# Performance work log

Measured on AMD Instinct MI355X. Metric: run time of the kernel, lower is better.

The kernel has to match this reference:

```python
import jax, jax.numpy as jnp
import numpy as np

NQ, NK, D = 8192, 8192, 256
NEG_INF = -1e30


def setup_inputs() -> dict:
    key = jax.random.key(0)
    kK, kV, kQ, kM = jax.random.split(key, 4)
    K = jax.random.normal(kK, (NK, D), dtype=jnp.float32)
    V = jax.random.normal(kV, (NK, D), dtype=jnp.float32)
    Q = jax.random.normal(kQ, (NQ, D), dtype=jnp.float32)
    m = jax.random.randint(kM, (NQ, NK), 0, 2) > 0  # bool mask, True = attend
    return {"K": K, "V": V, "Q": Q, "m": m}


def reference(K, V, Q, m):
    # affinity: scaled dot product with optional mask
    scale = 1.0 / jnp.sqrt(jnp.asarray(D, dtype=Q.dtype))
    QKt = jnp.einsum('qd,kd->qk', Q, K) * scale  # [NQ, NK]
    QKt = jnp.where(m, QKt, NEG_INF)
    # normalization: softmax over keys
    QKt_n = jax.nn.softmax(QKt, axis=-1)
    # weighted sum of values
    return QKt_n @ V  # [NQ, D]
```

## Files before the change

kernel.cpp:

```cpp
#include <hip/hip_runtime.h>
#include <stdint.h>
#include <stddef.h>

#define NQS 8192
#define NKS 8192
#define DS  256

typedef _Float16 half8 __attribute__((ext_vector_type(8)));
typedef _Float16 half4v __attribute__((ext_vector_type(4)));
typedef float floatx16 __attribute__((ext_vector_type(16)));
typedef float floatx4e __attribute__((ext_vector_type(4)));
typedef uint32_t uint32x4 __attribute__((ext_vector_type(4)));

#define MFMA32(A,B,C) __builtin_amdgcn_mfma_f32_32x32x16_f16(A,B,C,0,0,0)

#define GLOAD_LDS16(gp, lp) \
  __builtin_amdgcn_global_load_lds((const __attribute__((address_space(1))) void*)(gp), \
                                   (__attribute__((address_space(3))) void*)(lp), 16, 0, 0)

#define TILE_ELEMS 16384
#define SUB_ELEMS  8192

__global__ void detect_mask(const uint4* __restrict__ M, uint32_t* __restrict__ flag){
  __shared__ uint32_t s[256];
  uint32_t acc = 0;
  for (int i = threadIdx.x; i < 4096; i += 256){
    uint4 v = M[i];
    acc |= v.x | v.y | v.z | v.w;
  }
  s[threadIdx.x] = acc;
  __syncthreads();
  if (threadIdx.x == 0){
    uint32_t t = 0;
    for (int i = 0; i < 256; i++) t |= s[i];
    *flag = (t > 1u) ? 1u : 0u;
  }
}

__global__ void prep(const float* __restrict__ Qf, const float* __restrict__ K,
                     const float* __restrict__ V,
                     _Float16* __restrict__ Qh, _Float16* __restrict__ Kc,
                     _Float16* __restrict__ Vc){
  const int tid = threadIdx.x;
  if (blockIdx.x < 1024){
    size_t u = (size_t)blockIdx.x*256 + tid;
    const float4* src = (const float4*)(Qf + u*8);
    float4 a = src[0], b = src[1];
    half8 h = {(_Float16)a.x,(_Float16)a.y,(_Float16)a.z,(_Float16)a.w,
               (_Float16)b.x,(_Float16)b.y,(_Float16)b.z,(_Float16)b.w};
    *(half8*)(Qh + u*8) = h;
  } else if (blockIdx.x < 2048){
    int gid = (blockIdx.x - 1024)*256 + tid;
    int key = gid & 8191;
    int c   = gid >> 13;
    int kt = c >> 1, t = c & 1;
    const float4* s = (const float4*)(K + (size_t)key*DS + kt*16 + t*8);
    float4 x = s[0], y = s[1];
    half8 h = {(_Float16)x.x,(_Float16)x.y,(_Float16)x.z,(_Float16)x.w,
               (_Float16)y.x,(_Float16)y.y,(_Float16)y.z,(_Float16)y.w};
    int tile = key >> 6, mt = (key >> 5) & 1, k32 = key & 31;
    size_t off = (size_t)tile*TILE_ELEMS + (((mt*16 + kt)*2 + t)*32 + k32)*8;
    *(half8*)(Kc + off) = h;
  } else {
    int gid = (blockIdx.x - 2048)*256 + tid;
    int d32 = gid & 31;
    int t   = (gid >> 5) & 1;
    int nt  = (gid >> 6) & 7;
    int kkt = (gid >> 9) & 3;
    int tile = gid >> 11;
    int d = nt*32 + d32;
    int kb8 = tile*64 + kkt*16 + t*8;
    half8 h;
    #pragma unroll
    for (int j=0;j<8;j++) h[j] = (_Float16)V[(size_t)(kb8 + j)*DS + d];
    *(half8*)(Vc + (size_t)gid*8) = h;
  }
}

__global__ __launch_bounds__(256, 2) void attn_fwd(
  const _Float16* __restrict__ Qh, const _Float16* __restrict__ Kc,
  const _Float16* __restrict__ Vc, const uint8_t* __restrict__ Msk,
  const uint32_t* __restrict__ flag, _Float16* __restrict__ Oph,
  float* __restrict__ Lo)
{
  __shared__ _Float16 Kls[2][SUB_ELEMS];
  __shared__ _Float16 Vls[2][SUB_ELEMS];
  __shared__ uint8_t  Pk[16][128][8];

  const int tid  = threadIdx.x;
  const int w    = tid >> 6;
  const int lane = tid & 63;
  const int q32  = lane & 31;
  const int t    = lane >> 5;
  const int b    = blockIdx.x;
  const int kh   = b & 7;
  const int rb   = (b >> 3)*128;
  const int rowbase = rb + w*32;
  const int sub0 = kh << 5;
  const int kbase = kh << 10;

  const float kLog = 0.09016844005556021f;
  const float MFIX = 6.0f;

  const bool bm = (*flag != 0u);

  {
    const size_t base = (size_t)sub0 * SUB_ELEMS;
    #pragma unroll
    for (int j=0;j<4;j++){
      int c = w*4 + j;
      GLOAD_LDS16(Kc + base + c*512 + lane*8, &Kls[0][c*512]);
      GLOAD_LDS16(Vc + base + c*512 + lane*8, &Vls[0][c*512]);
    }
  }

  if (bm){
    const uint8_t* mrow = Msk + (size_t)(rb + (tid>>1))*NKS + kbase + (tid&1)*16;
    #pragma unroll 1
    for (int sp=0; sp<16; ++sp){
      uint32x4 e = __builtin_nontemporal_load((const uint32x4*)(mrow + sp*64));
      uint32x4 o = __builtin_nontemporal_load((const uint32x4*)(mrow + sp*64 + 32));
      #pragma unroll
      for (int q=0;q<4;q++){
        uint32_t xe = e[q], xo = o[q];
        uint8_t ne = (uint8_t)(((xe&0x000000FFu)?1u:0u)|((xe&0x0000FF00u)?2u:0u)|
                               ((xe&0x00FF0000u)?4u:0u)|((xe&0xFF000000u)?8u:0u));
        uint8_t no = (uint8_t)(((xo&0x000000FFu)?1u:0u)|((xo&0x0000FF00u)?2u:0u)|
                               ((xo&0x00FF0000u)?4u:0u)|((xo&0xFF000000u)?8u:0u));
        Pk[sp][tid>>1][(tid&1)*4 + q] = (uint8_t)(ne | (no << 4));
      }
    }
  } else {
    const uint32_t* M32 = (const uint32_t*)Msk;
    #pragma unroll 1
    for (int sp=0; sp<16; ++sp){
      uint32x4 e[4], o[4];
      #pragma unroll
      for (int jj=0;jj<4;jj++){
        const uint32_t* p = M32 + (size_t)(rb + jj*32 + (tid>>3))*NKS + kbase + sp*64 + (tid&7)*4;
        e[jj] = __builtin_nontemporal_load((const uint32x4*)p);
        o[jj] = __builtin_nontemporal_load((const uint32x4*)(p + 32));
      }
      #pragma unroll
      for (int jj=0;jj<4;jj++){
        uint8_t ne = (uint8_t)((e[jj][0]?1u:0u)|(e[jj][1]?2u:0u)|(e[jj][2]?4u:0u)|(e[jj][3]?8u:0u));
        uint8_t no = (uint8_t)((o[jj][0]?1u:0u)|(o[jj][1]?2u:0u)|(o[jj][2]?4u:0u)|(o[jj][3]?8u:0u));
        Pk[sp][jj*32 + (tid>>3)][tid&7] = (uint8_t)(ne | (no << 4));
      }
    }
  }

  half8 qf[16];
  {
    const _Float16* qrow = Qh + (size_t)(rowbase + q32)*DS;
    #pragma unroll
    for (int kt=0;kt<16;kt++)
      qf[kt] = *(const half8*)(qrow + kt*16 + t*8);
  }

  floatx16 O[8];
  #pragma unroll
  for (int nt=0;nt<8;nt++)
    #pragma unroll
    for (int i=0;i<16;i++) O[nt][i] = 0.f;
  float lsum = 0.f;

  __syncthreads();

  #pragma unroll 1
  for (int it=0; it<32; ++it){
    const int buf = it & 1;

    if (it < 31){
      const size_t base = (size_t)(sub0 + it + 1) * SUB_ELEMS;
      #pragma unroll
      for (int j=0;j<4;j++){
        int c = w*4 + j;
        GLOAD_LDS16(Kc + base + c*512 + lane*8, &Kls[buf^1][c*512]);
        GLOAD_LDS16(Vc + base + c*512 + lane*8, &Vls[buf^1][c*512]);
      }
    }

    const uint2 nq = *(const uint2*)&Pk[it>>1][w*32 + q32][0];
    const int sh = (it & 1) * 4;
    const uint32_t nib_s[4] = { (nq.x >> (8*t + sh))      & 0xFu,
                                (nq.x >> (16 + 8*t + sh)) & 0xFu,
                                (nq.y >> (8*t + sh))      & 0xFu,
                                (nq.y >> (16 + 8*t + sh)) & 0xFu };

    floatx16 S0, S1;
    #pragma unroll
    for (int i=0;i<16;i++){ S0[i]=0.f; S1[i]=0.f; }
    #pragma unroll
    for (int kt=0;kt<8;kt++){
      half8 kA = *(const half8*)&Kls[buf][((kt*2 + t)*32 + q32)*8];
      S0 = MFMA32(kA, qf[kt], S0);
    }
    #pragma unroll
    for (int kt=8;kt<16;kt++){
      half8 kA = *(const half8*)&Kls[buf][((kt*2 + t)*32 + q32)*8];
      S1 = MFMA32(kA, qf[kt], S1);
    }

    uint32_t pk[4][2];
    #pragma unroll
    for (int s=0;s<4;s++){
      float pv[4];
      #pragma unroll
      for (int rr=0;rr<4;rr++){
        int i = s*4 + rr;
        float e = __builtin_amdgcn_exp2f(__builtin_fmaf(S0[i]+S1[i], kLog, -MFIX));
        float p = ((nib_s[s] >> rr) & 1u) ? e : 0.f;
        lsum += p;
        pv[rr] = p;
      }
      pk[s][0] = __builtin_bit_cast(uint32_t, __builtin_amdgcn_cvt_pkrtz(pv[0], pv[1]));
      pk[s][1] = __builtin_bit_cast(uint32_t, __builtin_amdgcn_cvt_pkrtz(pv[2], pv[3]));
    }

    #pragma unroll
    for (int kt2=0; kt2<2; ++kt2){
      const int s_own  = kt2*2 + t;
      const int s_send = kt2*2 + (t^1);
      uint32_t r0 = __shfl_xor(__builtin_bit_cast(int, pk[s_send][0]), 32);
      uint32_t r1 = __shfl_xor(__builtin_bit_cast(int, pk[s_send][1]), 32);
      uint32_t lo0 = (t==0) ? pk[s_own][0] : r0;
      uint32_t lo1 = (t==0) ? pk[s_own][1] : r1;
      uint32_t hi0 = (t==0) ? r0 : pk[s_own][0];
      uint32_t hi1 = (t==0) ? r1 : pk[s_own][1];
      uint4 u = {lo0, lo1, hi0, hi1};
      half8 pa = __builtin_bit_cast(half8, u);
      #pragma unroll
      for (int nt=0;nt<8;nt++){
        half8 vB = *(const half8*)&Vls[buf][(((kt2*8+nt)*2 + t)*32 + q32)*8];
        O[nt] = MFMA32(pa, vB, O[nt]);
      }
    }

    __syncthreads();
  }

  lsum += __builtin_bit_cast(float, __shfl_xor(__builtin_bit_cast(int, lsum), 32));
  if (t == 0) __builtin_nontemporal_store(lsum, &Lo[(size_t)b*128 + w*32 + q32]);

  _Float16* ob = Oph + ((size_t)b*128 + w*32)*256;
  #pragma unroll
  for (int nt=0;nt<8;nt++){
    #pragma unroll
    for (int i=0;i<16;i++){
      int row = (i&3) + 8*(i>>2) + 4*t;
      __builtin_nontemporal_store((_Float16)O[nt][i], &ob[(size_t)row*256 + nt*32 + q32]);
    }
  }
}

__global__ void combine8(const _Float16* __restrict__ Oph, const float* __restrict__ Lo,
                         float* __restrict__ Out){
  int gid = blockIdx.x*256 + threadIdx.x;
  int row = gid >> 6;
  int c4  = (gid & 63) << 2;
  int g   = row >> 7, r = row & 127;

  float lt = 0.f;
  #pragma unroll
  for (int kh=0;kh<8;kh++) lt += __builtin_nontemporal_load(&Lo[(size_t)(g*8 + kh)*128 + r]);
  float li = 1.0f / lt;

  floatx4e acc = {0.f,0.f,0.f,0.f};
  #pragma unroll
  for (int kh=0;kh<8;kh++){
    half4v o = __builtin_nontemporal_load(
        (const half4v*)(Oph + ((size_t)(g*8 + kh)*128 + r)*256 + c4));
    acc[0] += (float)o[0]; acc[1] += (float)o[1];
    acc[2] += (float)o[2]; acc[3] += (float)o[3];
  }
  acc[0] *= li; acc[1] *= li; acc[2] *= li; acc[3] *= li;
  __builtin_nontemporal_store(acc, (floatx4e*)(Out + (size_t)row*DS + c4));
}

extern "C" void kernel_launch(void* const* d_in, const int* in_sizes, int n_in,
                              void* d_out, int out_size, void* d_ws, size_t ws_size,
                              hipStream_t stream){
  (void)in_sizes; (void)n_in; (void)out_size; (void)ws_size;
  const float*   K = (const float*)d_in[0];
  const float*   V = (const float*)d_in[1];
  const float*   Q = (const float*)d_in[2];
  const uint8_t* M = (const uint8_t*)d_in[3];
  float* Out = (float*)d_out;

  _Float16* Qh  = (_Float16*)d_ws;
  _Float16* Kc  = Qh + (size_t)NQS*DS;
  _Float16* Vc  = Kc + (size_t)NKS*DS;
  _Float16* Oph = Vc + (size_t)NKS*DS;
  float*    Lo  = (float*)(Oph + (size_t)512*128*256);
  uint32_t* flag = (uint32_t*)(Lo + 512*128);

  hipLaunchKernelGGL(detect_mask, dim3(1),    dim3(256), 0, stream, (const uint4*)M, flag);
  hipLaunchKernelGGL(prep,        dim3(3072), dim3(256), 0, stream, Q, K, V, Qh, Kc, Vc);
  hipLaunchKernelGGL(attn_fwd,    dim3(512),  dim3(256), 0, stream, Qh, Kc, Vc, M, flag, Oph, Lo);
  hipLaunchKernelGGL(combine8,    dim3(2048), dim3(256), 0, stream, Oph, Lo, Out);
}
```

Measured before the change: 467.4 us.

## Fold mask detection into prep, add MFMA priority hints, widen combine loads

The single-block mask-format detection kernel is merged into the prep kernel as an extra block, which removes one kernel launch. In attn_fwd the two QK MFMA chains are interleaved and wrapped in s_setprio hints, the mask nibble packing writes one 32-bit word instead of four bytes, and lsum is split into four accumulators. combine8 now handles 8 halves per thread with half the grid. These are several small latency and launch-overhead tweaks. They carry some risk of register-pressure changes in the main kernel.

```diff
diff --git a/kernel.cpp b/kernel.cpp
--- a/kernel.cpp
+++ b/kernel.cpp
@@ -21,36 +21,38 @@
 #define TILE_ELEMS 16384
 #define SUB_ELEMS  8192
 
-__global__ void detect_mask(const uint4* __restrict__ M, uint32_t* __restrict__ flag){
-  __shared__ uint32_t s[256];
-  uint32_t acc = 0;
-  for (int i = threadIdx.x; i < 4096; i += 256){
-    uint4 v = M[i];
-    acc |= v.x | v.y | v.z | v.w;
-  }
-  s[threadIdx.x] = acc;
-  __syncthreads();
-  if (threadIdx.x == 0){
-    uint32_t t = 0;
-    for (int i = 0; i < 256; i++) t |= s[i];
-    *flag = (t > 1u) ? 1u : 0u;
-  }
-}
-
 __global__ void prep(const float* __restrict__ Qf, const float* __restrict__ K,
-                     const float* __restrict__ V,
+                     const float* __restrict__ V, const uint8_t* __restrict__ Msk,
                      _Float16* __restrict__ Qh, _Float16* __restrict__ Kc,
-                     _Float16* __restrict__ Vc){
+                     _Float16* __restrict__ Vc, uint32_t* __restrict__ flag){
+  __shared__ uint32_t sdet[256];
   const int tid = threadIdx.x;
-  if (blockIdx.x < 1024){
-    size_t u = (size_t)blockIdx.x*256 + tid;
+  const int bid = blockIdx.x;
+  if (bid == 0){
+    const uint4* M4 = (const uint4*)Msk;
+    uint32_t acc = 0;
+    for (int i = tid; i < 4096; i += 256){
+      uint4 v = M4[i];
+      acc |= v.x | v.y | v.z | v.w;
+    }
+    sdet[tid] = acc;
+    __syncthreads();
+    if (tid == 0){
+      uint32_t t = 0;
+      for (int i = 0; i < 256; i++) t |= sdet[i];
+      *flag = (t > 1u) ? 1u : 0u;
+    }
+    return;
+  }
+  if (bid <= 1024){
+    size_t u = (size_t)(bid - 1)*256 + tid;
     const float4* src = (const float4*)(Qf + u*8);
     float4 a = src[0], b = src[1];
     half8 h = {(_Float16)a.x,(_Float16)a.y,(_Float16)a.z,(_Float16)a.w,
                (_Float16)b.x,(_Float16)b.y,(_Float16)b.z,(_Float16)b.w};
     *(half8*)(Qh + u*8) = h;
-  } else if (blockIdx.x < 2048){
-    int gid = (blockIdx.x - 1024)*256 + tid;
+  } else if (bid <= 2048){
+    int gid = (bid - 1025)*256 + tid;
     int key = gid & 8191;
     int c   = gid >> 13;
     int kt = c >> 1, t = c & 1;
@@ -62,7 +64,7 @@
     size_t off = (size_t)tile*TILE_ELEMS + (((mt*16 + kt)*2 + t)*32 + k32)*8;
     *(half8*)(Kc + off) = h;
   } else {
-    int gid = (blockIdx.x - 2048)*256 + tid;
+    int gid = (bid - 2049)*256 + tid;
     int d32 = gid & 31;
     int t   = (gid >> 5) & 1;
     int nt  = (gid >> 6) & 7;
@@ -120,15 +122,17 @@
     for (int sp=0; sp<16; ++sp){
       uint32x4 e = __builtin_nontemporal_load((const uint32x4*)(mrow + sp*64));
       uint32x4 o = __builtin_nontemporal_load((const uint32x4*)(mrow + sp*64 + 32));
+      uint32_t w4 = 0;
       #pragma unroll
       for (int q=0;q<4;q++){
         uint32_t xe = e[q], xo = o[q];
-        uint8_t ne = (uint8_t)(((xe&0x000000FFu)?1u:0u)|((xe&0x0000FF00u)?2u:0u)|
-                               ((xe&0x00FF0000u)?4u:0u)|((xe&0xFF000000u)?8u:0u));
-        uint8_t no = (uint8_t)(((xo&0x000000FFu)?1u:0u)|((xo&0x0000FF00u)?2u:0u)|
-                               ((xo&0x00FF0000u)?4u:0u)|((xo&0xFF000000u)?8u:0u));
-        Pk[sp][tid>>1][(tid&1)*4 + q] = (uint8_t)(ne | (no << 4));
-      }
+        uint32_t ne = ((xe&0x000000FFu)?1u:0u)|((xe&0x0000FF00u)?2u:0u)|
+                      ((xe&0x00FF0000u)?4u:0u)|((xe&0xFF000000u)?8u:0u);
+        uint32_t no = ((xo&0x000000FFu)?1u:0u)|((xo&0x0000FF00u)?2u:0u)|
+                      ((xo&0x00FF0000u)?4u:0u)|((xo&0xFF000000u)?8u:0u);
+        w4 |= (ne | (no << 4)) << (8*q);
+      }
+      *(uint32_t*)&Pk[sp][tid>>1][(tid&1)*4] = w4;
     }
   } else {
     const uint32_t* M32 = (const uint32_t*)Msk;
@@ -163,7 +167,7 @@
   for (int nt=0;nt<8;nt++)
     #pragma unroll
     for (int i=0;i<16;i++) O[nt][i] = 0.f;
-  float lsum = 0.f;
+  float ls[4] = {0.f, 0.f, 0.f, 0.f};
 
   __syncthreads();
 
@@ -191,16 +195,15 @@
     floatx16 S0, S1;
     #pragma unroll
     for (int i=0;i<16;i++){ S0[i]=0.f; S1[i]=0.f; }
+    __builtin_amdgcn_s_setprio(1);
     #pragma unroll
     for (int kt=0;kt<8;kt++){
-      half8 kA = *(const half8*)&Kls[buf][((kt*2 + t)*32 + q32)*8];
-      S0 = MFMA32(kA, qf[kt], S0);
-    }
-    #pragma unroll
-    for (int kt=8;kt<16;kt++){
-      half8 kA = *(const half8*)&Kls[buf][((kt*2 + t)*32 + q32)*8];
-      S1 = MFMA32(kA, qf[kt], S1);
-    }
+      half8 kA0 = *(const half8*)&Kls[buf][((kt*2 + t)*32 + q32)*8];
+      half8 kA1 = *(const half8*)&Kls[buf][(((kt+8)*2 + t)*32 + q32)*8];
+      S0 = MFMA32(kA0, qf[kt],   S0);
+      S1 = MFMA32(kA1, qf[kt+8], S1);
+    }
+    __builtin_amdgcn_s_setprio(0);
 
     uint32_t pk[4][2];
     #pragma unroll
@@ -211,7 +214,7 @@
         int i = s*4 + rr;
         float e = __builtin_amdgcn_exp2f(__builtin_fmaf(S0[i]+S1[i], kLog, -MFIX));
         float p = ((nib_s[s] >> rr) & 1u) ? e : 0.f;
-        lsum += p;
+        ls[s] += p;
         pv[rr] = p;
       }
       pk[s][0] = __builtin_bit_cast(uint32_t, __builtin_amdgcn_cvt_pkrtz(pv[0], pv[1]));
@@ -230,16 +233,19 @@
       uint32_t hi1 = (t==0) ? r1 : pk[s_own][1];
       uint4 u = {lo0, lo1, hi0, hi1};
       half8 pa = __builtin_bit_cast(half8, u);
+      __builtin_amdgcn_s_setprio(1);
       #pragma unroll
       for (int nt=0;nt<8;nt++){
         half8 vB = *(const half8*)&Vls[buf][(((kt2*8+nt)*2 + t)*32 + q32)*8];
         O[nt] = MFMA32(pa, vB, O[nt]);
       }
+      __builtin_amdgcn_s_setprio(0);
     }
 
     __syncthreads();
   }
 
+  float lsum = (ls[0] + ls[1]) + (ls[2] + ls[3]);
   lsum += __builtin_bit_cast(float, __shfl_xor(__builtin_bit_cast(int, lsum), 32));
   if (t == 0) __builtin_nontemporal_store(lsum, &Lo[(size_t)b*128 + w*32 + q32]);
 
@@ -257,8 +263,8 @@
 __global__ void combine8(const _Float16* __restrict__ Oph, const float* __restrict__ Lo,
                          float* __restrict__ Out){
   int gid = blockIdx.x*256 + threadIdx.x;
-  int row = gid >> 6;
-  int c4  = (gid & 63) << 2;
+  int row = gid >> 5;
+  int c8  = (gid & 31) << 3;
   int g   = row >> 7, r = row & 127;
 
   float lt = 0.f;
@@ -266,16 +272,18 @@
   for (int kh=0;kh<8;kh++) lt += __builtin_nontemporal_load(&Lo[(size_t)(g*8 + kh)*128 + r]);
   float li = 1.0f / lt;
 
-  floatx4e acc = {0.f,0.f,0.f,0.f};
+  float acc[8] = {0.f,0.f,0.f,0.f,0.f,0.f,0.f,0.f};
   #pragma unroll
   for (int kh=0;kh<8;kh++){
-    half4v o = __builtin_nontemporal_load(
-        (const half4v*)(Oph + ((size_t)(g*8 + kh)*128 + r)*256 + c4));
-    acc[0] += (float)o[0]; acc[1] += (float)o[1];
-    acc[2] += (float)o[2]; acc[3] += (float)o[3];
-  }
-  acc[0] *= li; acc[1] *= li; acc[2] *= li; acc[3] *= li;
-  __builtin_nontemporal_store(acc, (floatx4e*)(Out + (size_t)row*DS + c4));
+    half8 o = __builtin_nontemporal_load(
+        (const half8*)(Oph + ((size_t)(g*8 + kh)*128 + r)*256 + c8));
+    #pragma unroll
+    for (int j=0;j<8;j++) acc[j] += (float)o[j];
+  }
+  floatx4e a0 = {acc[0]*li, acc[1]*li, acc[2]*li, acc[3]*li};
+  floatx4e a1 = {acc[4]*li, acc[5]*li, acc[6]*li, acc[7]*li};
+  __builtin_nontemporal_store(a0, (floatx4e*)(Out + (size_t)row*DS + c8));
+  __builtin_nontemporal_store(a1, (floatx4e*)(Out + (size_t)row*DS + c8 + 4));
 }
 
 extern "C" void kernel_launch(void* const* d_in, const int* in_sizes, int n_in,
@@ -295,8 +303,7 @@
   float*    Lo  = (float*)(Oph + (size_t)512*128*256);
   uint32_t* flag = (uint32_t*)(Lo + 512*128);
 
-  hipLaunchKernelGGL(detect_mask, dim3(1),    dim3(256), 0, stream, (const uint4*)M, flag);
-  hipLaunchKernelGGL(prep,        dim3(3072), dim3(256), 0, stream, Q, K, V, Qh, Kc, Vc);
-  hipLaunchKernelGGL(attn_fwd,    dim3(512),  dim3(256), 0, stream, Qh, Kc, Vc, M, flag, Oph, Lo);
-  hipLaunchKernelGGL(combine8,    dim3(2048), dim3(256), 0, stream, Oph, Lo, Out);
+  hipLaunchKernelGGL(prep,     dim3(3073), dim3(256), 0, stream, Q, K, V, M, Qh, Kc, Vc, flag);
+  hipLaunchKernelGGL(attn_fwd, dim3(512),  dim3(256), 0, stream, Qh, Kc, Vc, M, flag, Oph, Lo);
+  hipLaunchKernelGGL(combine8, dim3(1024), dim3(256), 0, stream, Oph, Lo, Out);
 }
```

Result: no change. 471.8 us (+0.9%).
